# Kernel optimization log

Measured on AMD Instinct MI355X. Metric: run time of the kernel, lower is better.

Reference implementation:

```python
import jax, jax.numpy as jnp
import numpy as np

N_QUBITS = 10
DIM = 1 << N_QUBITS  # 1024

# Constant QFT matrix (PennyLane convention: F[j,k] = w^{jk}/sqrt(N), w = exp(2*pi*i/N),
# wire 0 = most significant bit). Symmetric, so state @ F == F @ state per sample.
_jk = (np.outer(np.arange(DIM), np.arange(DIM)) % DIM).astype(np.float64)
QFT_MAT = jnp.asarray((np.exp(2j * np.pi * _jk / DIM) / np.sqrt(DIM)).astype(np.complex64))


def _apply_1q(state, U, q):
    """Apply 2x2 gate U to wire q (wire 0 = MSB). state: [B, DIM] complex."""
    B = state.shape[0]
    left, right = 1 << q, 1 << (N_QUBITS - 1 - q)
    s = state.reshape(B, left, 2, right)
    s = jnp.einsum('ij,bajc->baic', U, s)
    return s.reshape(B, DIM)


def _apply_cnot(state, c, t):
    """CNOT with control c, target t (wire 0 = MSB)."""
    B = state.shape[0]
    a, b = (c, t) if c < t else (t, c)
    s = state.reshape(B, 1 << a, 2, 1 << (b - a - 1), 2, 1 << (N_QUBITS - 1 - b))
    ctrl_ax, tgt_ax = (2, 4) if c < t else (4, 2)
    s0 = jax.lax.index_in_dim(s, 0, ctrl_ax, keepdims=False)
    s1 = jax.lax.index_in_dim(s, 1, ctrl_ax, keepdims=False)
    ta = tgt_ax - 1 if tgt_ax > ctrl_ax else tgt_ax  # target axis after squeezing ctrl
    s1 = jnp.flip(s1, axis=ta)  # X on target when control == 1
    s = jnp.stack([s0, s1], axis=ctrl_ax)
    return s.reshape(B, DIM)


def _rx(t):
    c = jnp.cos(t / 2).astype(jnp.complex64)
    s = (-1j * jnp.sin(t / 2)).astype(jnp.complex64)
    return jnp.stack([jnp.stack([c, s]), jnp.stack([s, c])])


def _ry(t):
    c = jnp.cos(t / 2).astype(jnp.complex64)
    s = jnp.sin(t / 2).astype(jnp.complex64)
    return jnp.stack([jnp.stack([c, -s]), jnp.stack([s, c])])


def _rz(t):
    e = jnp.exp(-0.5j * t.astype(jnp.complex64))
    z = jnp.zeros((), jnp.complex64)
    return jnp.stack([jnp.stack([e, z]), jnp.stack([z, jnp.conj(e)])])


def _forward(x, weights):
    B = x.shape[0]
    # Pad/truncate is a no-op here (x already [B, DIM]); normalize as in the module.
    nrm = jnp.linalg.norm(x, axis=-1, keepdims=True)
    xn = x / jnp.maximum(nrm, 1e-8)
    state = xn.astype(jnp.complex64)  # AmplitudeEmbedding (already unit-norm)
    for q in range(N_QUBITS):
        state = _apply_1q(state, _rx(weights[q, 0]), q)
    for q in range(N_QUBITS):
        state = _apply_1q(state, _ry(weights[q, 1]), q)
    for q in range(N_QUBITS):
        state = _apply_1q(state, _rz(weights[q, 2]), q)
    for q in range(N_QUBITS):
        state = _apply_cnot(state, q, (q + 1) % N_QUBITS)
    for q in range(N_QUBITS):
        state = _apply_1q(state, _ry(weights[q, 3]), q)
    state = state @ QFT_MAT  # QFT (symmetric matrix)
    ex, ey, ez = [], [], []
    for q in range(N_QUBITS):
        s = state.reshape(B, 1 << q, 2, 1 << (N_QUBITS - 1 - q))
        s0, s1 = s[:, :, 0, :], s[:, :, 1, :]
        cross = jnp.sum(jnp.conj(s0) * s1, axis=(1, 2))
        ex.append(2.0 * jnp.real(cross))                # <X_q>
        ey.append(2.0 * jnp.imag(cross))                # <Y_q>
        ez.append(jnp.sum(jnp.abs(s0) ** 2 - jnp.abs(s1) ** 2, axis=(1, 2)))  # <Z_q>
    return jnp.stack(ex + ey + ez, axis=1).astype(jnp.float32)  # [B, 3*N_QUBITS]


def setup_inputs() -> dict:
    key = jax.random.key(0)
    kx, kw = jax.random.split(key)
    x = jax.random.normal(kx, (8192, 1024), dtype=jnp.float32)
    weights = jax.random.normal(kw, (10, 4), dtype=jnp.float32) * 0.01
    return {"x": x, "weights": weights}


def reference(x, weights):
    return _forward(x, weights)
```

## Files before the change

kernel.cpp:

```cpp
#include <hip/hip_runtime.h>


typedef _Float16 half8_t __attribute__((ext_vector_type(8)));
typedef _Float16 half4_t __attribute__((ext_vector_type(4)));
typedef float floatx4 __attribute__((ext_vector_type(4)));

#define GLB_CAST(p) ((const __attribute__((address_space(1))) void*)(p))
#define LDS_CAST(p) ((__attribute__((address_space(3))) void*)(p))

__global__ __launch_bounds__(256) void prep_kernel(const float* __restrict__ w,
                                                   const float* __restrict__ x,
                                                   _Float16* __restrict__ Wh,
                                                   _Float16* __restrict__ Xh)
{
    __shared__ float smem[2048 + 88];
    const int tid = threadIdx.x;

    if (blockIdx.x >= 1024) {
        float* wsum = smem;
        const int b = blockIdx.x - 1024;
        float4 v = ((const float4*)(x + (size_t)b * 1024))[tid];
        float ss = v.x*v.x + v.y*v.y + v.z*v.z + v.w*v.w;
        #pragma unroll
        for (int off = 32; off; off >>= 1) ss += __shfl_down(ss, off);
        if ((tid & 63) == 0) wsum[tid >> 6] = ss;
        __syncthreads();
        float scale = 1.0f / fmaxf(sqrtf(wsum[0] + wsum[1] + wsum[2] + wsum[3]), 1e-8f);
        half4_t h;
        h[0] = (_Float16)(v.x * scale);
        h[1] = (_Float16)(v.y * scale);
        h[2] = (_Float16)(v.z * scale);
        h[3] = (_Float16)(v.w * scale);
        ((half4_t*)(Xh + (size_t)b * 1024))[tid] = h;
        return;
    }

    float* sr  = smem;
    float* si  = smem + 1024;
    float* wc  = smem + 2048;
    float* wsn = smem + 2088;
    const int jb = blockIdx.x;

    if (tid < 40) {
        float t = w[tid] * 0.5f;
        wc[tid]  = cosf(t);
        wsn[tid] = sinf(t);
    }
    for (int i = tid; i < 1024; i += 256) { sr[i] = (i == jb) ? 1.0f : 0.0f; si[i] = 0.0f; }
    __syncthreads();

    for (int layer = 0; layer < 4; ++layer) {
        if (layer == 3) {
            for (int q = 0; q < 10; ++q) {
                int mc = 1 << (9 - q);
                int mt = 1 << (9 - ((q + 1) % 10));
                for (int p = tid; p < 512; p += 256) {
                    int i0 = ((p & ~(mt - 1)) << 1) | (p & (mt - 1));
                    if (i0 & mc) {
                        int i1 = i0 | mt;
                        float tr = sr[i0]; sr[i0] = sr[i1]; sr[i1] = tr;
                        float ti = si[i0]; si[i0] = si[i1]; si[i1] = ti;
                    }
                }
                __syncthreads();
            }
        }
        int wi = (layer == 3) ? 3 : layer;
        for (int q = 0; q < 10; ++q) {
            float c = wc[q * 4 + wi], s = wsn[q * 4 + wi];
            float u00r, u00i, u01r, u01i, u10r, u10i, u11r, u11i;
            if (layer == 0) {
                u00r=c; u00i=0; u01r=0; u01i=-s; u10r=0; u10i=-s; u11r=c; u11i=0;
            } else if (layer == 2) {
                u00r=c; u00i=-s; u01r=0; u01i=0; u10r=0; u10i=0; u11r=c; u11i=s;
            } else {
                u00r=c; u00i=0; u01r=-s; u01i=0; u10r=s; u10i=0; u11r=c; u11i=0;
            }
            int m = 1 << (9 - q);
            for (int p = tid; p < 512; p += 256) {
                int i0 = ((p & ~(m - 1)) << 1) | (p & (m - 1));
                int i1 = i0 | m;
                float ar = sr[i0], ai = si[i0], br = sr[i1], bi = si[i1];
                sr[i0] = u00r*ar - u00i*ai + u01r*br - u01i*bi;
                si[i0] = u00r*ai + u00i*ar + u01r*bi + u01i*br;
                sr[i1] = u10r*ar - u10i*ai + u11r*br - u11i*bi;
                si[i1] = u10r*ai + u10i*ar + u11r*bi + u11i*br;
            }
            __syncthreads();
        }
    }

    for (int i = tid; i < 1024; i += 256) {
        int r = (int)(__brev((unsigned)i) >> 22);
        if (r > i) {
            float tr = sr[i]; sr[i] = sr[r]; sr[r] = tr;
            float ti = si[i]; si[i] = si[r]; si[r] = ti;
        }
    }
    __syncthreads();
    for (int st = 1; st <= 10; ++st) {
        int hf = 1 << (st - 1);
        float astep = 6.28318530717958647f / (float)(1 << st);
        for (int p = tid; p < 512; p += 256) {
            int j2 = p & (hf - 1);
            int i0 = ((p >> (st - 1)) << st) | j2;
            int i1 = i0 + hf;
            float ang = astep * (float)j2;
            float sw, cw;
            __sincosf(ang, &sw, &cw);
            float br2 = sr[i1], bi2 = si[i1];
            float tr = cw*br2 - sw*bi2;
            float ti = cw*bi2 + sw*br2;
            float ur = sr[i0], ui = si[i0];
            sr[i0] = ur + tr; si[i0] = ui + ti;
            sr[i1] = ur - tr; si[i1] = ui - ti;
        }
        __syncthreads();
    }
    for (int k = tid; k < 1024; k += 256) {
        Wh[(size_t)jb * 2048 + 2*k]     = (_Float16)(sr[k] * 0.03125f);
        Wh[(size_t)jb * 2048 + 2*k + 1] = (_Float16)(si[k] * 0.03125f);
    }
}

__global__ __launch_bounds__(256) void transpose_kernel(const _Float16* __restrict__ Wh,
                                                        _Float16* __restrict__ Bt)
{
    __shared__ _Float16 tile[32][33];
    const int bx = blockIdx.x;
    const int by = blockIdx.y;
    const int tx = threadIdx.x;
    const int ty = threadIdx.y;
    #pragma unroll
    for (int i = 0; i < 4; ++i) {
        int r = ty + 8*i;
        tile[r][tx] = Wh[(size_t)(by*32 + r) * 2048 + bx*32 + tx];
    }
    __syncthreads();
    #pragma unroll
    for (int i = 0; i < 4; ++i) {
        int r = ty + 8*i;
        Bt[(size_t)(bx*32 + r) * 1024 + by*32 + tx] = tile[tx][r];
    }
}

__global__ __launch_bounds__(256, 2) void gemm_kernel(const _Float16* __restrict__ A,
                                                      const _Float16* __restrict__ Bt,
                                                      _Float16* __restrict__ C)
{
    __shared__ __align__(16) _Float16 As[128][64];
    __shared__ __align__(16) _Float16 Bs[128][64];
    const int tid  = threadIdx.x;
    const int wave = tid >> 6;
    const int lane = tid & 63;
    const int m0 = blockIdx.y * 128;
    const int n0 = blockIdx.x * 128;

    const int srow = lane >> 3;
    const int schk = (lane & 7) ^ srow;
    const _Float16* gA = A  + (size_t)(m0 + 32*wave + srow) * 1024 + schk * 8;
    const _Float16* gB = Bt + (size_t)(n0 + 32*wave + srow) * 1024 + schk * 8;
    _Float16* lA = &As[0][0] + wave*2048 + lane*8;
    _Float16* lB = &Bs[0][0] + wave*2048 + lane*8;

    const int fr = lane & 15;
    const int fc = lane >> 4;
    const int sx = fr & 7;
    const int wm = (wave >> 1) * 64;
    const int wn = (wave & 1) * 64;

    floatx4 acc[4][4];
    #pragma unroll
    for (int i = 0; i < 4; ++i)
        #pragma unroll
        for (int j = 0; j < 4; ++j)
            acc[i][j] = (floatx4){0.f, 0.f, 0.f, 0.f};

    for (int kt = 0; kt < 16; ++kt) {
        #pragma unroll
        for (int t = 0; t < 4; ++t) {
            __builtin_amdgcn_global_load_lds(GLB_CAST(gA + (size_t)t*8*1024), LDS_CAST(lA + t*512), 16, 0, 0);
            __builtin_amdgcn_global_load_lds(GLB_CAST(gB + (size_t)t*8*1024), LDS_CAST(lB + t*512), 16, 0, 0);
        }
        gA += 64; gB += 64;
        __syncthreads();
        #pragma unroll
        for (int kh = 0; kh < 2; ++kh) {
            half8_t af[4], bf[4];
            #pragma unroll
            for (int i = 0; i < 4; ++i)
                af[i] = *(const half8_t*)&As[wm + i*16 + fr][((kh*4 + fc) ^ sx) * 8];
            #pragma unroll
            for (int i = 0; i < 4; ++i)
                bf[i] = *(const half8_t*)&Bs[wn + i*16 + fr][((kh*4 + fc) ^ sx) * 8];
            #pragma unroll
            for (int mi = 0; mi < 4; ++mi)
                #pragma unroll
                for (int ni = 0; ni < 4; ++ni)
                    acc[mi][ni] = __builtin_amdgcn_mfma_f32_16x16x32_f16(af[mi], bf[ni], acc[mi][ni], 0, 0, 0);
        }
        __syncthreads();
    }

    #pragma unroll
    for (int mi = 0; mi < 4; ++mi) {
        #pragma unroll
        for (int r = 0; r < 4; ++r) {
            int row = m0 + wm + mi*16 + fc*4 + r;
            _Float16* cp = C + (size_t)row * 2048 + n0 + wn + fr;
            #pragma unroll
            for (int ni = 0; ni < 4; ++ni)
                cp[ni*16] = (_Float16)acc[mi][ni][r];
        }
    }
}

__device__ __forceinline__ float wred(float v) {
    v += __shfl_xor(v, 1);
    v += __shfl_xor(v, 2);
    v += __shfl_xor(v, 4);
    v += __shfl_xor(v, 8);
    v += __shfl_xor(v, 16);
    v += __shfl_xor(v, 32);
    return v;
}

__global__ __launch_bounds__(128, 2) void expect_kernel(const _Float16* __restrict__ Sh,
                                                        float* __restrict__ out)
{
    __shared__ __align__(16) float buf[2][2048];
    const int tid = threadIdx.x;
    const int w = tid >> 6, l = tid & 63;
    const int row = blockIdx.x * 2 + w;
    float* bw = buf[w];

    const _Float16* src = Sh + (size_t)row * 2048 + l * 32;
    float2 c[16];
    #pragma unroll
    for (int t = 0; t < 4; ++t) {
        half8_t v = ((const half8_t*)src)[t];
        #pragma unroll
        for (int u = 0; u < 4; ++u)
            c[t*4 + u] = make_float2((float)v[2*u], (float)v[2*u + 1]);
    }

    #pragma unroll
    for (int j = 0; j < 8; ++j) {
        int su = l*8 + (j ^ (l & 7));
        ((float4*)bw)[su] = make_float4(c[2*j].x, c[2*j].y, c[2*j+1].x, c[2*j+1].y);
    }

    float P2s = 0.f;
    #pragma unroll
    for (int i = 0; i < 16; ++i)
        P2s += c[i].x*c[i].x + c[i].y*c[i].y;

    float outv = 0.f;

    #pragma unroll
    for (int p = 0; p < 4; ++p) {
        const int m = 1 << p;
        const int q = 9 - p;
        float rr = 0.f, ii = 0.f, zz = 0.f;
        #pragma unroll
        for (int i = 0; i < 16; ++i) {
            if (i & m) continue;
            const int j = i | m;
            rr += c[i].x*c[j].x + c[i].y*c[j].y;
            ii += c[i].x*c[j].y - c[i].y*c[j].x;
            zz += (c[i].x*c[i].x + c[i].y*c[i].y) - (c[j].x*c[j].x + c[j].y*c[j].y);
        }
        rr = wred(rr);
        ii = wred(ii);
        zz = wred(zz);
        outv = (l == q)      ? 2.f*rr : outv;
        outv = (l == 10 + q) ? 2.f*ii : outv;
        outv = (l == 20 + q) ? zz     : outv;
    }

    #pragma unroll
    for (int e = 0; e < 6; ++e) {
        const int q = 5 - e;
        const int part = l ^ (1 << e);
        const int mybit = (l >> e) & 1;
        const float sgn = mybit ? -1.f : 1.f;
        const int j0 = mybit ? 4 : 0;
        float rr = 0.f, ii = 0.f;
        #pragma unroll
        for (int j = 0; j < 4; ++j) {
            const int su = part*8 + ((j0 + j) ^ (part & 7));
            float4 f = ((const float4*)bw)[su];
            const float2 a0 = c[2*j],     a1 = c[2*j + 1];
            const float2 b0 = c[2*j + 8], b1 = c[2*j + 9];
            const float m0x = mybit ? b0.x : a0.x;
            const float m0y = mybit ? b0.y : a0.y;
            const float m1x = mybit ? b1.x : a1.x;
            const float m1y = mybit ? b1.y : a1.y;
            rr += m0x*f.x + m0y*f.y;
            ii += m0x*f.y - m0y*f.x;
            rr += m1x*f.z + m1y*f.w;
            ii += m1x*f.w - m1y*f.z;
        }
        float rr_s = wred(rr);
        float ii_s = wred(sgn * ii);
        float zz_s = wred(sgn * P2s);
        outv = (l == q)      ? 2.f*rr_s : outv;
        outv = (l == 10 + q) ? 2.f*ii_s : outv;
        outv = (l == 20 + q) ? zz_s     : outv;
    }

    if (l < 30)
        out[(size_t)row * 30 + l] = outv;
}

extern "C" void kernel_launch(void* const* d_in, const int* in_sizes, int n_in,
                              void* d_out, int out_size, void* d_ws, size_t ws_size,
                              hipStream_t stream) {
    const float* x = (const float*)d_in[0];
    const float* w = (const float*)d_in[1];
    float* out = (float*)d_out;
    char* ws = (char*)d_ws;
    _Float16* Wh = (_Float16*)(ws);
    _Float16* Bt = (_Float16*)(ws + ((size_t)4  << 20));
    _Float16* Xh = (_Float16*)(ws + ((size_t)8  << 20));
    _Float16* Sh = (_Float16*)(ws + ((size_t)24 << 20));

    prep_kernel<<<9216, 256, 0, stream>>>(w, x, Wh, Xh);
    transpose_kernel<<<dim3(64, 32), dim3(32, 8), 0, stream>>>(Wh, Bt);
    gemm_kernel<<<dim3(16, 64), 256, 0, stream>>>(Xh, Bt, Sh);
    expect_kernel<<<4096, 128, 0, stream>>>(Sh, out);
}
```

Before: 172.1 us.

## Fuse gate pairs and radix-4 FFT in prep kernel with padded LDS

The per-block state-vector simulation in the prep kernel now applies two single-qubit gates per LDS pass, so each thread holds four amplitudes in registers. It replaces the ten sequential CNOT passes plus the bit-reversal with a single computed permutation gather into a second buffer. The FFT is rewritten as radix-4 stages, and LDS indexing gets padding to reduce bank conflicts. This halves the number of barriers and LDS round trips, at the cost of more LDS space and a more intricate index mapping that must match the original gate ordering.

```diff
diff --git a/kernel.cpp b/kernel.cpp
--- a/kernel.cpp
+++ b/kernel.cpp
@@ -7,13 +7,32 @@
 
 #define GLB_CAST(p) ((const __attribute__((address_space(1))) void*)(p))
 #define LDS_CAST(p) ((__attribute__((address_space(3))) void*)(p))
+
+#define IDX(k) ((k) + ((k) >> 5))
+
+__device__ __forceinline__ void gate2(int type, float c, float s,
+                                      float& ar, float& ai, float& br, float& bi)
+{
+    float nar, nai, nbr, nbi;
+    if (type == 0) {
+        nar =  c*ar + s*bi;  nai =  c*ai - s*br;
+        nbr =  s*ai + c*br;  nbi = -s*ar + c*bi;
+    } else if (type == 2) {
+        nar =  c*ar + s*ai;  nai =  c*ai - s*ar;
+        nbr =  c*br - s*bi;  nbi =  c*bi + s*br;
+    } else {
+        nar =  c*ar - s*br;  nai =  c*ai - s*bi;
+        nbr =  s*ar + c*br;  nbi =  s*ai + c*bi;
+    }
+    ar = nar; ai = nai; br = nbr; bi = nbi;
+}
 
 __global__ __launch_bounds__(256) void prep_kernel(const float* __restrict__ w,
                                                    const float* __restrict__ x,
                                                    _Float16* __restrict__ Wh,
                                                    _Float16* __restrict__ Xh)
 {
-    __shared__ float smem[2048 + 88];
+    __shared__ float smem[4304];
     const int tid = threadIdx.x;
 
     if (blockIdx.x >= 1024) {
@@ -36,9 +55,11 @@
     }
 
     float* sr  = smem;
-    float* si  = smem + 1024;
-    float* wc  = smem + 2048;
-    float* wsn = smem + 2088;
+    float* si  = smem + 1056;
+    float* sr2 = smem + 2112;
+    float* si2 = smem + 3168;
+    float* wc  = smem + 4224;
+    float* wsn = smem + 4264;
     const int jb = blockIdx.x;
 
     if (tid < 40) {
@@ -46,81 +67,115 @@
         wc[tid]  = cosf(t);
         wsn[tid] = sinf(t);
     }
-    for (int i = tid; i < 1024; i += 256) { sr[i] = (i == jb) ? 1.0f : 0.0f; si[i] = 0.0f; }
+    #pragma unroll
+    for (int u = 0; u < 4; ++u) {
+        int k = tid + 256*u;
+        sr[IDX(k)] = (k == jb) ? 1.0f : 0.0f;
+        si[IDX(k)] = 0.0f;
+    }
     __syncthreads();
 
-    for (int layer = 0; layer < 4; ++layer) {
-        if (layer == 3) {
-            for (int q = 0; q < 10; ++q) {
-                int mc = 1 << (9 - q);
-                int mt = 1 << (9 - ((q + 1) % 10));
-                for (int p = tid; p < 512; p += 256) {
-                    int i0 = ((p & ~(mt - 1)) << 1) | (p & (mt - 1));
-                    if (i0 & mc) {
-                        int i1 = i0 | mt;
-                        float tr = sr[i0]; sr[i0] = sr[i1]; sr[i1] = tr;
-                        float ti = si[i0]; si[i0] = si[i1]; si[i1] = ti;
-                    }
-                }
-                __syncthreads();
+    for (int layer = 0; layer < 3; ++layer) {
+        for (int pp = 0; pp < 5; ++pp) {
+            const int p  = 2*pp;
+            const int m1 = 1 << p, m2 = 2 << p;
+            const int base = ((tid >> p) << (p + 2)) | (tid & (m1 - 1));
+            const int iA = IDX(base), iB = IDX(base + m1);
+            const int iC = IDX(base + m2), iD = IDX(base + m1 + m2);
+            float Ar = sr[iA], Ai = si[iA], Br = sr[iB], Bi = si[iB];
+            float Cr = sr[iC], Ci = si[iC], Dr = sr[iD], Di = si[iD];
+            {
+                float c = wc[(9 - p)*4 + layer], s = wsn[(9 - p)*4 + layer];
+                gate2(layer, c, s, Ar, Ai, Br, Bi);
+                gate2(layer, c, s, Cr, Ci, Dr, Di);
             }
-        }
-        int wi = (layer == 3) ? 3 : layer;
-        for (int q = 0; q < 10; ++q) {
-            float c = wc[q * 4 + wi], s = wsn[q * 4 + wi];
-            float u00r, u00i, u01r, u01i, u10r, u10i, u11r, u11i;
-            if (layer == 0) {
-                u00r=c; u00i=0; u01r=0; u01i=-s; u10r=0; u10i=-s; u11r=c; u11i=0;
-            } else if (layer == 2) {
-                u00r=c; u00i=-s; u01r=0; u01i=0; u10r=0; u10i=0; u11r=c; u11i=s;
-            } else {
-                u00r=c; u00i=0; u01r=-s; u01i=0; u10r=s; u10i=0; u11r=c; u11i=0;
+            {
+                float c = wc[(8 - p)*4 + layer], s = wsn[(8 - p)*4 + layer];
+                gate2(layer, c, s, Ar, Ai, Cr, Ci);
+                gate2(layer, c, s, Br, Bi, Dr, Di);
             }
-            int m = 1 << (9 - q);
-            for (int p = tid; p < 512; p += 256) {
-                int i0 = ((p & ~(m - 1)) << 1) | (p & (m - 1));
-                int i1 = i0 | m;
-                float ar = sr[i0], ai = si[i0], br = sr[i1], bi = si[i1];
-                sr[i0] = u00r*ar - u00i*ai + u01r*br - u01i*bi;
-                si[i0] = u00r*ai + u00i*ar + u01r*bi + u01i*br;
-                sr[i1] = u10r*ar - u10i*ai + u11r*br - u11i*bi;
-                si[i1] = u10r*ai + u10i*ar + u11r*bi + u11i*br;
-            }
+            sr[iA] = Ar; si[iA] = Ai; sr[iB] = Br; si[iB] = Bi;
+            sr[iC] = Cr; si[iC] = Ci; sr[iD] = Dr; si[iD] = Di;
             __syncthreads();
         }
     }
 
-    for (int i = tid; i < 1024; i += 256) {
-        int r = (int)(__brev((unsigned)i) >> 22);
-        if (r > i) {
-            float tr = sr[i]; sr[i] = sr[r]; sr[r] = tr;
-            float ti = si[i]; si[i] = si[r]; si[r] = ti;
-        }
+    #pragma unroll
+    for (int u = 0; u < 4; ++u) {
+        int k = tid + 256*u;
+        int m = (int)(__brev((unsigned)k) >> 22);
+        #pragma unroll
+        for (int q = 9; q >= 0; --q) {
+            const int pc = (q == 9) ? 0 : 9 - q;
+            const int pt = (q == 9) ? 9 : 8 - q;
+            m ^= ((m >> pc) & 1) << pt;
+        }
+        sr2[IDX(k)] = sr[IDX(m)];
+        si2[IDX(k)] = si[IDX(m)];
     }
     __syncthreads();
-    for (int st = 1; st <= 10; ++st) {
-        int hf = 1 << (st - 1);
-        float astep = 6.28318530717958647f / (float)(1 << st);
-        for (int p = tid; p < 512; p += 256) {
-            int j2 = p & (hf - 1);
-            int i0 = ((p >> (st - 1)) << st) | j2;
-            int i1 = i0 + hf;
-            float ang = astep * (float)j2;
-            float sw, cw;
-            __sincosf(ang, &sw, &cw);
-            float br2 = sr[i1], bi2 = si[i1];
-            float tr = cw*br2 - sw*bi2;
-            float ti = cw*bi2 + sw*br2;
-            float ur = sr[i0], ui = si[i0];
-            sr[i0] = ur + tr; si[i0] = ui + ti;
-            sr[i1] = ur - tr; si[i1] = ui - ti;
-        }
-        __syncthreads();
-    }
-    for (int k = tid; k < 1024; k += 256) {
-        Wh[(size_t)jb * 2048 + 2*k]     = (_Float16)(sr[k] * 0.03125f);
-        Wh[(size_t)jb * 2048 + 2*k + 1] = (_Float16)(si[k] * 0.03125f);
-    }
+
+    for (int pp = 0; pp < 5; ++pp) {
+        const int p  = 2*pp;
+        const int m1 = 1 << p, m2 = 2 << p;
+        const int base = ((tid >> p) << (p + 2)) | (tid & (m1 - 1));
+        const int iA = IDX(base), iB = IDX(base + m1);
+        const int iC = IDX(base + m2), iD = IDX(base + m1 + m2);
+        const float* rsrc = (pp == 0) ? sr2 : sr;
+        const float* isrc = (pp == 0) ? si2 : si;
+        float Ar = rsrc[iA], Ai = isrc[iA], Br = rsrc[iB], Bi = isrc[iB];
+        float Cr = rsrc[iC], Ci = isrc[iC], Dr = rsrc[iD], Di = isrc[iD];
+        {
+            float c = wc[p*4 + 3], s = wsn[p*4 + 3];
+            gate2(1, c, s, Ar, Ai, Br, Bi);
+            gate2(1, c, s, Cr, Ci, Dr, Di);
+        }
+        {
+            float c = wc[(p + 1)*4 + 3], s = wsn[(p + 1)*4 + 3];
+            gate2(1, c, s, Ar, Ai, Cr, Ci);
+            gate2(1, c, s, Br, Bi, Dr, Di);
+        }
+        sr[iA] = Ar; si[iA] = Ai; sr[iB] = Br; si[iB] = Bi;
+        sr[iC] = Cr; si[iC] = Ci; sr[iD] = Dr; si[iD] = Di;
+        __syncthreads();
+    }
+
+    for (int sp = 0; sp < 5; ++sp) {
+        const int st = 2*sp + 1;
+        const int hf = 1 << (st - 1);
+        const int j2 = tid & (hf - 1);
+        const int i0 = ((tid >> (st - 1)) << (st + 1)) | j2;
+        const int iA = IDX(i0), iB = IDX(i0 + hf);
+        const int iC = IDX(i0 + 2*hf), iD = IDX(i0 + 3*hf);
+        float Ar = sr[iA], Ai = si[iA], Br = sr[iB], Bi = si[iB];
+        float Cr = sr[iC], Ci = si[iC], Dr = sr[iD], Di = si[iD];
+        const float th1 = (6.28318530717958647f / (float)(1 << st)) * (float)j2;
+        float s1, c1, s2, c2;
+        __sincosf(th1, &s1, &c1);
+        __sincosf(th1 * 0.5f, &s2, &c2);
+        float t1r = c1*Br - s1*Bi, t1i = c1*Bi + s1*Br;
+        float Apr = Ar + t1r, Api = Ai + t1i;
+        float Bpr = Ar - t1r, Bpi = Ai - t1i;
+        float t2r = c1*Dr - s1*Di, t2i = c1*Di + s1*Dr;
+        float Cpr = Cr + t2r, Cpi = Ci + t2i;
+        float Dpr = Cr - t2r, Dpi = Ci - t2i;
+        float u1r = c2*Cpr - s2*Cpi, u1i = c2*Cpi + s2*Cpr;
+        sr[iA] = Apr + u1r; si[iA] = Api + u1i;
+        sr[iC] = Apr - u1r; si[iC] = Api - u1i;
+        float u2r = c2*Dpr - s2*Dpi, u2i = c2*Dpi + s2*Dpr;
+        sr[iB] = Bpr - u2i; si[iB] = Bpi + u2r;
+        sr[iD] = Bpr + u2i; si[iD] = Bpi - u2r;
+        __syncthreads();
+    }
+
+    half8_t v;
+    #pragma unroll
+    for (int u = 0; u < 4; ++u) {
+        const int k = 4*tid + u;
+        v[2*u]     = (_Float16)(sr[IDX(k)] * 0.03125f);
+        v[2*u + 1] = (_Float16)(si[IDX(k)] * 0.03125f);
+    }
+    ((half8_t*)(Wh + (size_t)jb * 2048))[tid] = v;
 }
 
 __global__ __launch_bounds__(256) void transpose_kernel(const _Float16* __restrict__ Wh,
```

After: 155.3 us. 9.8% less time.
